# Performance work log

Measured on AMD Instinct MI355X. Metric: run time of the kernel, lower is better.

Reference implementation:

```python
import jax, jax.numpy as jnp
import numpy as np

N = 50000
E = 1600000
F_IN = 128
F_OUT = 64
NEG_SLOPE = 0.2


def setup_inputs() -> dict:
    key = jax.random.key(0)
    k1, k2, k3, k4, k5, k6 = jax.random.split(key, 6)
    x = jax.random.normal(k1, (N, F_IN), dtype=jnp.float32)
    edge_index = jax.random.randint(k2, (2, E), 0, N, dtype=jnp.int64)
    # GATConv params (heads=1): glorot-ish scale
    W = jax.random.normal(k3, (F_IN, F_OUT), dtype=jnp.float32) * (1.0 / np.sqrt(F_IN))
    att_src = jax.random.normal(k4, (F_OUT,), dtype=jnp.float32) * (1.0 / np.sqrt(F_OUT))
    att_dst = jax.random.normal(k5, (F_OUT,), dtype=jnp.float32) * (1.0 / np.sqrt(F_OUT))
    bias = jnp.zeros((F_OUT,), dtype=jnp.float32)
    return {"x": x, "edge_index": edge_index, "W": W, "att_src": att_src, "att_dst": att_dst, "bias": bias}


def _gat_forward(x, edge_index, W, att_src, att_dst, bias):
    n = x.shape[0]
    # add self loops (PyG GATConv default)
    loops = jnp.arange(n, dtype=edge_index.dtype)
    src = jnp.concatenate([edge_index[0], loops])  # [E+N]
    dst = jnp.concatenate([edge_index[1], loops])  # [E+N]

    h = x @ W                                      # [N, F_OUT]
    a_src = h @ att_src                            # [N]
    a_dst = h @ att_dst                            # [N]

    e = a_src[src] + a_dst[dst]                    # [E+N]
    e = jnp.where(e > 0, e, NEG_SLOPE * e)         # LeakyReLU(0.2)

    # softmax over edges grouped by destination node
    e_max = jax.ops.segment_max(e, dst, num_segments=n)     # [N]
    e_exp = jnp.exp(e - e_max[dst])                          # [E+N]
    e_sum = jax.ops.segment_sum(e_exp, dst, num_segments=n)  # [N]
    alpha = e_exp / e_sum[dst]                               # [E+N]

    msg = h[src] * alpha[:, None]                            # [E+N, F_OUT]
    out = jax.ops.segment_sum(msg, dst, num_segments=n)      # [N, F_OUT]
    out = out + bias
    return jax.nn.relu(out)


def reference(x, edge_index, W, att_src, att_dst, bias):
    return _gat_forward(x, edge_index, W, att_src, att_dst, bias)
```

## Files before the change

kernel.cpp:

```cpp
#include <hip/hip_runtime.h>

#define NN 50000
#define NE 1600000
#define FIN 128
#define FOUT 64
#define SLOPE 0.2f

#define NB   1563
#define NPB  32
#define CAPB 1536
#define FBLK 261
#define CHC4 1536
#define GBLK 782
#define LW   136

typedef unsigned int u32;
typedef short short8 __attribute__((ext_vector_type(8)));
typedef float f32x4 __attribute__((ext_vector_type(4)));

__device__ __forceinline__ unsigned short f2bf(float f) {
    u32 u = __float_as_uint(f);
    u += 0x7FFFu + ((u >> 16) & 1u);
    return (unsigned short)(u >> 16);
}
__device__ __forceinline__ float bf2f(unsigned short s) {
    return __uint_as_float(((u32)s) << 16);
}

union FusedLds {
    struct { unsigned short xs[64 * LW]; unsigned short Wt[64 * LW]; } g;
    struct { int lc[NB]; int lb[NB]; } f;
};

__global__ __launch_bounds__(256) void fused_k(
        const float* __restrict__ x, const float* __restrict__ W,
        const float* __restrict__ att_s, const float* __restrict__ att_d,
        const int* __restrict__ ei, int* __restrict__ bcur,
        u32* __restrict__ staging, unsigned short* __restrict__ h,
        float* __restrict__ a_src, float* __restrict__ a_dst) {
    __shared__ FusedLds L;
    const int tid = threadIdx.x;

    if (blockIdx.x < FBLK) {
        int* lc = L.f.lc; int* lb = L.f.lb;
        for (int j = tid; j < NB; j += 256) lc[j] = 0;
        __syncthreads();
        const int4* sd4 = (const int4*)(ei + NE);
        const int4* ss4 = (const int4*)ei;
        const int lo = blockIdx.x * CHC4, hi = min(NE / 4, lo + CHC4);
        for (int i = lo + tid; i < hi; i += 256) {
            int4 d = sd4[i];
            atomicAdd(&lc[d.x >> 5], 1);
            atomicAdd(&lc[d.y >> 5], 1);
            atomicAdd(&lc[d.z >> 5], 1);
            atomicAdd(&lc[d.w >> 5], 1);
        }
        __syncthreads();
        for (int j = tid; j < NB; j += 256) {
            int c = lc[j];
            lb[j] = c ? atomicAdd(&bcur[j], c) : 0;
        }
        __syncthreads();
        for (int j = tid; j < NB; j += 256) lc[j] = 0;
        __syncthreads();
        for (int i = lo + tid; i < hi; i += 256) {
            int4 d = sd4[i];
            int4 s = ss4[i];
            int b, pos;
            b = d.x >> 5; pos = lb[b] + atomicAdd(&lc[b], 1);
            if (pos < CAPB) staging[b * CAPB + pos] = (u32)s.x | ((u32)(d.x & 31) << 16);
            b = d.y >> 5; pos = lb[b] + atomicAdd(&lc[b], 1);
            if (pos < CAPB) staging[b * CAPB + pos] = (u32)s.y | ((u32)(d.y & 31) << 16);
            b = d.z >> 5; pos = lb[b] + atomicAdd(&lc[b], 1);
            if (pos < CAPB) staging[b * CAPB + pos] = (u32)s.z | ((u32)(d.z & 31) << 16);
            b = d.w >> 5; pos = lb[b] + atomicAdd(&lc[b], 1);
            if (pos < CAPB) staging[b * CAPB + pos] = (u32)s.w | ((u32)(d.w & 31) << 16);
        }
    } else {
        unsigned short* xs = L.g.xs;
        unsigned short* Wt = L.g.Wt;
        const int node0 = (blockIdx.x - FBLK) * 64;
        for (int i = tid; i < 128 * 16; i += 256) {
            int k = i >> 4, f = (i & 15) * 4;
            float4 w4 = ((const float4*)W)[i];
            Wt[(f + 0) * LW + k] = f2bf(w4.x);
            Wt[(f + 1) * LW + k] = f2bf(w4.y);
            Wt[(f + 2) * LW + k] = f2bf(w4.z);
            Wt[(f + 3) * LW + k] = f2bf(w4.w);
        }
        const float4* x4 = (const float4*)x;
        #pragma unroll
        for (int p = 0; p < 8; ++p) {
            int row = (tid >> 5) + p * 8, c = tid & 31;
            int node = node0 + row;
            float4 v = (node < NN) ? x4[(size_t)node * 32 + c]
                                   : make_float4(0.f, 0.f, 0.f, 0.f);
            ushort4 b;
            b.x = f2bf(v.x); b.y = f2bf(v.y); b.z = f2bf(v.z); b.w = f2bf(v.w);
            *(ushort4*)(xs + row * LW + c * 4) = b;
        }
        __syncthreads();

        const int wv = tid >> 6, lane = tid & 63;
        const int q = lane >> 4, mr = lane & 15;
        f32x4 acc[4] = {{0,0,0,0},{0,0,0,0},{0,0,0,0},{0,0,0,0}};
        const unsigned short* arow = xs + (wv * 16 + mr) * LW;
        #pragma unroll
        for (int ks = 0; ks < 4; ++ks) {
            short8 a = *(const short8*)(arow + ks * 32 + q * 8);
            #pragma unroll
            for (int nt = 0; nt < 4; ++nt) {
                short8 b = *(const short8*)(Wt + (nt * 16 + mr) * LW + ks * 32 + q * 8);
                acc[nt] = __builtin_amdgcn_mfma_f32_16x16x32_bf16(a, b, acc[nt], 0, 0, 0);
            }
        }
        float atts[4], attd[4];
        #pragma unroll
        for (int nt = 0; nt < 4; ++nt) {
            atts[nt] = att_s[nt * 16 + mr];
            attd[nt] = att_d[nt * 16 + mr];
        }
        #pragma unroll
        for (int r = 0; r < 4; ++r) {
            int node = node0 + wv * 16 + q * 4 + r;
            float ps = 0.f, pd = 0.f;
            #pragma unroll
            for (int nt = 0; nt < 4; ++nt) {
                float v = acc[nt][r];
                if (node < NN) h[(size_t)node * 64 + nt * 16 + mr] = f2bf(v);
                ps += v * atts[nt];
                pd += v * attd[nt];
            }
            #pragma unroll
            for (int off = 8; off > 0; off >>= 1) {
                ps += __shfl_xor(ps, off);
                pd += __shfl_xor(pd, off);
            }
            if (mr == 0 && node < NN) { a_src[node] = ps; a_dst[node] = pd; }
        }
    }
}

__global__ __launch_bounds__(256) void agg_k(
        const u32* __restrict__ staging, const int* __restrict__ bcur,
        const float* __restrict__ a_src, const float* __restrict__ a_dst,
        const u32* __restrict__ h32, const float* __restrict__ bias,
        float* __restrict__ out) {
    const int bkt = blockIdx.x;
    const int node0 = bkt << 5;
    if (node0 >= NN) return;
    const int nNodes = min(NPB, NN - node0);
    const int bsize = min(bcur[bkt], CAPB);
    const u32* stg = staging + bkt * CAPB;
    const int tid = threadIdx.x, wv = tid >> 6, lane = tid & 63;

    __shared__ u32 pk[CAPB];
    __shared__ unsigned short ssrc[CAPB];
    __shared__ int lcnt[NPB];
    __shared__ int lbase[NPB + 1];
    __shared__ int lcur[NPB];
    float* evals = (float*)pk;

    for (int j = tid; j < bsize; j += 256) pk[j] = stg[j];
    if (tid < NPB) lcnt[tid] = 0;
    __syncthreads();
    for (int j = tid; j < bsize; j += 256)
        atomicAdd(&lcnt[pk[j] >> 16], 1);
    __syncthreads();
    if (tid < 64) {
        int v = (tid < NPB) ? lcnt[tid] : 0;
        #pragma unroll
        for (int off = 1; off < NPB; off <<= 1) {
            int u = __shfl_up(v, off);
            if (tid >= off) v += u;
        }
        if (tid < NPB) lbase[tid + 1] = v;
        if (tid == 0) lbase[0] = 0;
    }
    if (tid >= 64 && tid < 64 + NPB) lcur[tid - 64] = 0;
    __syncthreads();
    for (int j = tid; j < bsize; j += 256) {
        u32 w = pk[j];
        int ld = w >> 16;
        int pos = lbase[ld] + atomicAdd(&lcur[ld], 1);
        ssrc[pos] = (unsigned short)(w & 0xFFFFu);
    }
    __syncthreads();

    const int half = lane >> 5, hl = lane & 31;
    for (int p = wv; p < 16; p += 4) {
        const int ln = p * 2 + half;
        if (ln >= nNodes) continue;
        const int n = node0 + ln;
        const int st = lbase[ln], deg = lbase[ln + 1] - st;
        const float ad = a_dst[n];
        float es = a_src[n] + ad; es = es > 0.f ? es : SLOPE * es;
        const float ps = __expf(es);
        float sum = 0.f;
        for (int j = hl; j < deg; j += 32) {
            int s = ssrc[st + j];
            float e = a_src[s] + ad; e = e > 0.f ? e : SLOPE * e;
            float pe = __expf(e);
            evals[st + j] = pe;
            sum += pe;
        }
        #pragma unroll
        for (int off = 16; off > 0; off >>= 1) sum += __shfl_xor(sum, off);
        const float inv = 1.f / (sum + ps);
        u32 hs = h32[(size_t)n * 32 + hl];
        float ax = ps * bf2f((unsigned short)(hs & 0xFFFFu));
        float ay = ps * bf2f((unsigned short)(hs >> 16));
        #pragma unroll 4
        for (int j = 0; j < deg; ++j) {
            int s = ssrc[st + j];
            float ev = evals[st + j];
            u32 hv = h32[(size_t)s * 32 + hl];
            ax += ev * bf2f((unsigned short)(hv & 0xFFFFu));
            ay += ev * bf2f((unsigned short)(hv >> 16));
        }
        float2 bv = ((const float2*)bias)[hl];
        float vx = ax * inv + bv.x;
        float vy = ay * inv + bv.y;
        float2 o;
        o.x = vx > 0.f ? vx : 0.f;
        o.y = vy > 0.f ? vy : 0.f;
        ((float2*)out)[(size_t)n * 32 + hl] = o;
    }
}

extern "C" void kernel_launch(void* const* d_in, const int* in_sizes, int n_in,
                              void* d_out, int out_size, void* d_ws, size_t ws_size,
                              hipStream_t stream) {
    const float* x     = (const float*)d_in[0];
    const int*   ei    = (const int*)d_in[1];
    const float* W     = (const float*)d_in[2];
    const float* att_s = (const float*)d_in[3];
    const float* att_d = (const float*)d_in[4];
    const float* bias  = (const float*)d_in[5];
    float* out = (float*)d_out;

    unsigned short* h = (unsigned short*)d_ws;
    float* a_src  = (float*)(h + (size_t)NN * 64);
    float* a_dst  = a_src + NN;
    int*   bcur   = (int*)(a_dst + NN);
    u32*   staging = (u32*)(bcur + 2048);

    hipMemsetAsync(bcur, 0, NB * sizeof(int), stream);

    fused_k<<<FBLK + GBLK, 256, 0, stream>>>(x, W, att_s, att_d, ei, bcur,
                                             staging, h, a_src, a_dst);
    agg_k<<<NB, 256, 0, stream>>>(staging, bcur, a_src, a_dst,
                                  (const u32*)h, bias, out);
}
```

Baseline: 151.8 us.

## Use global atomics for bucketing, register-load x tiles, widen aggregation per lane

The edge bucketing drops the two-pass LDS histogram and takes staging slots directly with one global atomicAdd per edge, using twice as many smaller blocks. The GEMM branch loads x straight into MFMA A-fragments in registers and no longer stages it through LDS. The aggregation kernel maps 16 lanes per node, each handling 4 features as ushort4, and unrolls the neighbor loop by 4 to expose more independent gathers. Global per-edge atomics add contention on 1563 counters and make the slot order nondeterministic, in exchange for fewer passes and barriers.

Result: slower. 363.1 us (+139.1%).

```diff
diff --git a/kernel.cpp b/kernel.cpp
--- a/kernel.cpp
+++ b/kernel.cpp
@@ -9,8 +9,8 @@
 #define NB   1563
 #define NPB  32
 #define CAPB 1536
-#define FBLK 261
-#define CHC4 1536
+#define FBLK 522
+#define CHC4 768
 #define GBLK 782
 #define LW   136
 
@@ -26,11 +26,6 @@
 __device__ __forceinline__ float bf2f(unsigned short s) {
     return __uint_as_float(((u32)s) << 16);
 }
-
-union FusedLds {
-    struct { unsigned short xs[64 * LW]; unsigned short Wt[64 * LW]; } g;
-    struct { int lc[NB]; int lb[NB]; } f;
-};
 
 __global__ __launch_bounds__(256) void fused_k(
         const float* __restrict__ x, const float* __restrict__ W,
@@ -38,47 +33,27 @@
         const int* __restrict__ ei, int* __restrict__ bcur,
         u32* __restrict__ staging, unsigned short* __restrict__ h,
         float* __restrict__ a_src, float* __restrict__ a_dst) {
-    __shared__ FusedLds L;
+    __shared__ unsigned short Wt[64 * LW];
     const int tid = threadIdx.x;
 
     if (blockIdx.x < FBLK) {
-        int* lc = L.f.lc; int* lb = L.f.lb;
-        for (int j = tid; j < NB; j += 256) lc[j] = 0;
-        __syncthreads();
         const int4* sd4 = (const int4*)(ei + NE);
         const int4* ss4 = (const int4*)ei;
         const int lo = blockIdx.x * CHC4, hi = min(NE / 4, lo + CHC4);
         for (int i = lo + tid; i < hi; i += 256) {
             int4 d = sd4[i];
-            atomicAdd(&lc[d.x >> 5], 1);
-            atomicAdd(&lc[d.y >> 5], 1);
-            atomicAdd(&lc[d.z >> 5], 1);
-            atomicAdd(&lc[d.w >> 5], 1);
-        }
-        __syncthreads();
-        for (int j = tid; j < NB; j += 256) {
-            int c = lc[j];
-            lb[j] = c ? atomicAdd(&bcur[j], c) : 0;
-        }
-        __syncthreads();
-        for (int j = tid; j < NB; j += 256) lc[j] = 0;
-        __syncthreads();
-        for (int i = lo + tid; i < hi; i += 256) {
-            int4 d = sd4[i];
             int4 s = ss4[i];
             int b, pos;
-            b = d.x >> 5; pos = lb[b] + atomicAdd(&lc[b], 1);
+            b = d.x >> 5; pos = atomicAdd(&bcur[b], 1);
             if (pos < CAPB) staging[b * CAPB + pos] = (u32)s.x | ((u32)(d.x & 31) << 16);
-            b = d.y >> 5; pos = lb[b] + atomicAdd(&lc[b], 1);
+            b = d.y >> 5; pos = atomicAdd(&bcur[b], 1);
             if (pos < CAPB) staging[b * CAPB + pos] = (u32)s.y | ((u32)(d.y & 31) << 16);
-            b = d.z >> 5; pos = lb[b] + atomicAdd(&lc[b], 1);
+            b = d.z >> 5; pos = atomicAdd(&bcur[b], 1);
             if (pos < CAPB) staging[b * CAPB + pos] = (u32)s.z | ((u32)(d.z & 31) << 16);
-            b = d.w >> 5; pos = lb[b] + atomicAdd(&lc[b], 1);
+            b = d.w >> 5; pos = atomicAdd(&bcur[b], 1);
             if (pos < CAPB) staging[b * CAPB + pos] = (u32)s.w | ((u32)(d.w & 31) << 16);
         }
     } else {
-        unsigned short* xs = L.g.xs;
-        unsigned short* Wt = L.g.Wt;
         const int node0 = (blockIdx.x - FBLK) * 64;
         for (int i = tid; i < 128 * 16; i += 256) {
             int k = i >> 4, f = (i & 15) * 4;
@@ -88,30 +63,37 @@
             Wt[(f + 2) * LW + k] = f2bf(w4.z);
             Wt[(f + 3) * LW + k] = f2bf(w4.w);
         }
-        const float4* x4 = (const float4*)x;
-        #pragma unroll
-        for (int p = 0; p < 8; ++p) {
-            int row = (tid >> 5) + p * 8, c = tid & 31;
-            int node = node0 + row;
-            float4 v = (node < NN) ? x4[(size_t)node * 32 + c]
-                                   : make_float4(0.f, 0.f, 0.f, 0.f);
-            ushort4 b;
-            b.x = f2bf(v.x); b.y = f2bf(v.y); b.z = f2bf(v.z); b.w = f2bf(v.w);
-            *(ushort4*)(xs + row * LW + c * 4) = b;
-        }
-        __syncthreads();
 
         const int wv = tid >> 6, lane = tid & 63;
         const int q = lane >> 4, mr = lane & 15;
+        const int row = node0 + wv * 16 + mr;
+        const bool valid = row < NN;
+        const float4* x4 = (const float4*)x;
+
+        short8 afr[4];
+        #pragma unroll
+        for (int ks = 0; ks < 4; ++ks) {
+            float4 f0 = make_float4(0.f, 0.f, 0.f, 0.f), f1 = f0;
+            if (valid) {
+                f0 = x4[(size_t)row * 32 + ks * 8 + q * 2];
+                f1 = x4[(size_t)row * 32 + ks * 8 + q * 2 + 1];
+            }
+            short8 a;
+            a[0] = (short)f2bf(f0.x); a[1] = (short)f2bf(f0.y);
+            a[2] = (short)f2bf(f0.z); a[3] = (short)f2bf(f0.w);
+            a[4] = (short)f2bf(f1.x); a[5] = (short)f2bf(f1.y);
+            a[6] = (short)f2bf(f1.z); a[7] = (short)f2bf(f1.w);
+            afr[ks] = a;
+        }
+        __syncthreads();
+
         f32x4 acc[4] = {{0,0,0,0},{0,0,0,0},{0,0,0,0},{0,0,0,0}};
-        const unsigned short* arow = xs + (wv * 16 + mr) * LW;
         #pragma unroll
         for (int ks = 0; ks < 4; ++ks) {
-            short8 a = *(const short8*)(arow + ks * 32 + q * 8);
             #pragma unroll
             for (int nt = 0; nt < 4; ++nt) {
                 short8 b = *(const short8*)(Wt + (nt * 16 + mr) * LW + ks * 32 + q * 8);
-                acc[nt] = __builtin_amdgcn_mfma_f32_16x16x32_bf16(a, b, acc[nt], 0, 0, 0);
+                acc[nt] = __builtin_amdgcn_mfma_f32_16x16x32_bf16(afr[ks], b, acc[nt], 0, 0, 0);
             }
         }
         float atts[4], attd[4];
@@ -144,11 +126,10 @@
 __global__ __launch_bounds__(256) void agg_k(
         const u32* __restrict__ staging, const int* __restrict__ bcur,
         const float* __restrict__ a_src, const float* __restrict__ a_dst,
-        const u32* __restrict__ h32, const float* __restrict__ bias,
+        const ushort4* __restrict__ h4, const float* __restrict__ bias,
         float* __restrict__ out) {
     const int bkt = blockIdx.x;
     const int node0 = bkt << 5;
-    if (node0 >= NN) return;
     const int nNodes = min(NPB, NN - node0);
     const int bsize = min(bcur[bkt], CAPB);
     const u32* stg = staging + bkt * CAPB;
@@ -187,9 +168,11 @@
     }
     __syncthreads();
 
-    const int half = lane >> 5, hl = lane & 31;
-    for (int p = wv; p < 16; p += 4) {
-        const int ln = p * 2 + half;
+    const int q = lane >> 4, ql = lane & 15;
+    const float4 b4 = ((const float4*)bias)[ql];
+    #pragma unroll
+    for (int rnd = 0; rnd < 2; ++rnd) {
+        const int ln = rnd * 16 + wv * 4 + q;
         if (ln >= nNodes) continue;
         const int n = node0 + ln;
         const int st = lbase[ln], deg = lbase[ln + 1] - st;
@@ -197,34 +180,52 @@
         float es = a_src[n] + ad; es = es > 0.f ? es : SLOPE * es;
         const float ps = __expf(es);
         float sum = 0.f;
-        for (int j = hl; j < deg; j += 32) {
+        for (int j = ql; j < deg; j += 16) {
             int s = ssrc[st + j];
             float e = a_src[s] + ad; e = e > 0.f ? e : SLOPE * e;
             float pe = __expf(e);
             evals[st + j] = pe;
             sum += pe;
         }
-        #pragma unroll
-        for (int off = 16; off > 0; off >>= 1) sum += __shfl_xor(sum, off);
+        sum += __shfl_xor(sum, 8); sum += __shfl_xor(sum, 4);
+        sum += __shfl_xor(sum, 2); sum += __shfl_xor(sum, 1);
         const float inv = 1.f / (sum + ps);
-        u32 hs = h32[(size_t)n * 32 + hl];
-        float ax = ps * bf2f((unsigned short)(hs & 0xFFFFu));
-        float ay = ps * bf2f((unsigned short)(hs >> 16));
-        #pragma unroll 4
-        for (int j = 0; j < deg; ++j) {
+
+        ushort4 hs = h4[(size_t)n * 16 + ql];
+        float a0 = ps * bf2f(hs.x), a1 = ps * bf2f(hs.y);
+        float a2 = ps * bf2f(hs.z), a3 = ps * bf2f(hs.w);
+        int j = 0;
+        for (; j + 4 <= deg; j += 4) {
+            int s0 = ssrc[st + j], s1 = ssrc[st + j + 1];
+            int s2 = ssrc[st + j + 2], s3 = ssrc[st + j + 3];
+            float e0 = evals[st + j], e1 = evals[st + j + 1];
+            float e2 = evals[st + j + 2], e3 = evals[st + j + 3];
+            ushort4 v0 = h4[(size_t)s0 * 16 + ql];
+            ushort4 v1 = h4[(size_t)s1 * 16 + ql];
+            ushort4 v2 = h4[(size_t)s2 * 16 + ql];
+            ushort4 v3 = h4[(size_t)s3 * 16 + ql];
+            a0 += e0 * bf2f(v0.x); a1 += e0 * bf2f(v0.y);
+            a2 += e0 * bf2f(v0.z); a3 += e0 * bf2f(v0.w);
+            a0 += e1 * bf2f(v1.x); a1 += e1 * bf2f(v1.y);
+            a2 += e1 * bf2f(v1.z); a3 += e1 * bf2f(v1.w);
+            a0 += e2 * bf2f(v2.x); a1 += e2 * bf2f(v2.y);
+            a2 += e2 * bf2f(v2.z); a3 += e2 * bf2f(v2.w);
+            a0 += e3 * bf2f(v3.x); a1 += e3 * bf2f(v3.y);
+            a2 += e3 * bf2f(v3.z); a3 += e3 * bf2f(v3.w);
+        }
+        for (; j < deg; ++j) {
             int s = ssrc[st + j];
             float ev = evals[st + j];
-            u32 hv = h32[(size_t)s * 32 + hl];
-            ax += ev * bf2f((unsigned short)(hv & 0xFFFFu));
-            ay += ev * bf2f((unsigned short)(hv >> 16));
-        }
-        float2 bv = ((const float2*)bias)[hl];
-        float vx = ax * inv + bv.x;
-        float vy = ay * inv + bv.y;
-        float2 o;
-        o.x = vx > 0.f ? vx : 0.f;
-        o.y = vy > 0.f ? vy : 0.f;
-        ((float2*)out)[(size_t)n * 32 + hl] = o;
+            ushort4 hv = h4[(size_t)s * 16 + ql];
+            a0 += ev * bf2f(hv.x); a1 += ev * bf2f(hv.y);
+            a2 += ev * bf2f(hv.z); a3 += ev * bf2f(hv.w);
+        }
+        float4 o;
+        o.x = a0 * inv + b4.x; o.x = o.x > 0.f ? o.x : 0.f;
+        o.y = a1 * inv + b4.y; o.y = o.y > 0.f ? o.y : 0.f;
+        o.z = a2 * inv + b4.z; o.z = o.z > 0.f ? o.z : 0.f;
+        o.w = a3 * inv + b4.w; o.w = o.w > 0.f ? o.w : 0.f;
+        ((float4*)out)[(size_t)n * 16 + ql] = o;
     }
 }
 
@@ -250,5 +251,5 @@
     fused_k<<<FBLK + GBLK, 256, 0, stream>>>(x, W, att_s, att_d, ei, bcur,
                                              staging, h, a_src, a_dst);
     agg_k<<<NB, 256, 0, stream>>>(staging, bcur, a_src, a_dst,
-                                  (const u32*)h, bias, out);
-}
+                                  (const ushort4*)h, bias, out);
+}
```
